# Kernel tuning notes

Hardware: AMD Instinct MI355X
Metric: run time of the kernel (lower is better)

Reference implementation:

```python
import jax, jax.numpy as jnp
import numpy as np

DIM = 512      # model dim
HEADS = 8      # attention heads
WS = 256       # window_size
G = 32         # num_global_tokens
SPARSITY = 0.3 # fraction of entries masked out per row by the sparsity controller


def setup_inputs() -> dict:
    key = jax.random.key(0)
    ks = jax.random.split(key, 7)
    b, n = 4, 8192
    x = jax.random.normal(ks[0], (b, n, DIM), dtype=jnp.float32)
    w_qkv = jax.random.normal(ks[1], (DIM, 3 * DIM), dtype=jnp.float32) * (DIM ** -0.5)
    w_out = jax.random.normal(ks[2], (DIM, DIM), dtype=jnp.float32) * (DIM ** -0.5)
    b_out = jnp.zeros((DIM,), dtype=jnp.float32)
    local_bias = jax.random.normal(ks[3], (HEADS, WS, WS), dtype=jnp.float32)
    global_param = jax.random.normal(ks[4], (HEADS, G, WS), dtype=jnp.float32)
    gate = jax.random.normal(ks[5], (HEADS,), dtype=jnp.float32)
    return {"x": x, "w_qkv": w_qkv, "w_out": w_out, "b_out": b_out,
            "local_bias": local_bias, "global_param": global_param, "gate": gate}


def reference(x, w_qkv, w_out, b_out, local_bias, global_param, gate):
    b, n, _ = x.shape
    h, ws, g = HEADS, WS, G
    d = DIM // h
    w = n // ws  # number of windows
    scale = DIM ** -0.5

    qkv = x @ w_qkv                      # [b, n, 3*dim]
    q, k, v = jnp.split(qkv, 3, axis=-1)

    def to_win(t):  # [b, n, dim] -> [b, h, w, ws, d]
        return t.reshape(b, n, h, d).transpose(0, 2, 1, 3).reshape(b, h, w, ws, d)

    q, k, v = to_win(q), to_win(k), to_win(v)

    # windowed local attention with learned per-window additive bias
    local = jnp.einsum('bhwnd,bhwmd->bhwnm', q, k) * scale   # [b,h,w,ws,ws]
    local = local + local_bias[None, :, None]                # bias broadcast over b, w

    # global-token attention term built from window-averaged q/k
    q_mean = q.mean(axis=2)  # [b,h,ws,d]
    k_mean = k.mean(axis=2)  # [b,h,ws,d]
    global_q = jnp.einsum('hgn,bhnd->bhgd', global_param, q_mean)      # [b,h,g,d]
    global_scores = jnp.einsum('bhgd,bhmd->bhgm', global_q, k_mean) * scale  # [b,h,g,ws]
    global_bias = global_scores.mean(axis=2)                            # [b,h,ws]

    # sparsity controller: learned per-head gate combines local + global,
    # then top-k row sparsification keeps (1-sparsity) of entries pre-softmax
    gate_h = jax.nn.sigmoid(gate)[None, :, None, None, None]
    scores = local + gate_h * global_bias[:, :, None, None, :]          # [b,h,w,ws,ws]
    k_keep = int(ws * (1.0 - SPARSITY))
    thresh = jax.lax.top_k(scores, k_keep)[0][..., -1:]                 # kth largest per row
    scores = jnp.where(scores >= thresh, scores, jnp.float32(-1e9))

    attn = jax.nn.softmax(scores, axis=-1)
    out = jnp.einsum('bhwnm,bhwmd->bhwnd', attn, v)                     # [b,h,w,ws,d]
    out = out.reshape(b, h, n, d).transpose(0, 2, 1, 3).reshape(b, n, DIM)
    return out @ w_out + b_out
```

## Files before the change

### kernel.cpp

```cpp
#include <hip/hip_runtime.h>

#define NN    8192
#define WSZ   256
#define KKEEP 179
#define SCALE 0.044194173824159216f

typedef __attribute__((ext_vector_type(8))) __bf16 bf16x8;
typedef __attribute__((ext_vector_type(4))) short  s16x4;
typedef __attribute__((ext_vector_type(8))) short  s16x8;
typedef __attribute__((ext_vector_type(4))) float  f32x4;

struct Split3 { short h, m, l; };
__device__ __forceinline__ Split3 split3(float x)
{
    unsigned u  = __float_as_uint(x);
    unsigned hb = ((u + 0x7FFFu + ((u >> 16) & 1u)) >> 16) << 16;
    float r = x - __uint_as_float(hb);
    unsigned ur = __float_as_uint(r);
    unsigned mb = ((ur + 0x7FFFu + ((ur >> 16) & 1u)) >> 16) << 16;
    float r2 = r - __uint_as_float(mb);
    unsigned lr = __float_as_uint(r2);
    unsigned lb = (lr + 0x7FFFu + ((lr >> 16) & 1u)) >> 16;
    Split3 s;
    s.h = (short)(hb >> 16);
    s.m = (short)(mb >> 16);
    s.l = (short)(lb & 0xFFFFu);
    return s;
}

__global__ __launch_bounds__(256) void splitw_kernel(const float* __restrict__ W,
                                                     int K, int N,
                                                     short* __restrict__ h,
                                                     short* __restrict__ m,
                                                     short* __restrict__ l)
{
    int idx = blockIdx.x * 256 + threadIdx.x;
    if (idx >= K * N) return;
    int k = idx / N, n = idx - k * N;
    Split3 s = split3(W[idx]);
    size_t o = (size_t)n * K + k;
    h[o] = s.h; m[o] = s.m; l[o] = s.l;
}

__global__ __launch_bounds__(256, 2) void gemm_mfma(const float* __restrict__ A, int lda,
                                                    const short* __restrict__ BTh,
                                                    const short* __restrict__ BTm,
                                                    const short* __restrict__ BTl,
                                                    const float* __restrict__ bias,
                                                    float* __restrict__ C, int ldc,
                                                    int qk_cols)
{
    __shared__ __align__(16) short Asm[3][128 * 40];
    __shared__ __align__(16) short Bsm[3][128 * 40];

    const int t       = threadIdx.x;
    const int lane    = t & 63;
    const int wave    = t >> 6;
    const int wr      = wave >> 1;
    const int wc      = wave & 1;
    const int rowBase = blockIdx.y * 128;
    const int colBase = blockIdx.x * 128;
    const int pstart  = (colBase < qk_cols) ? 0 : 3;

    const int sa[6] = {2, 0, 1, 1, 0, 0};
    const int sb[6] = {0, 2, 1, 0, 1, 0};

    const int fn = lane & 15;
    const int fq = (lane >> 4) * 8;

    f32x4 acc[4][4] = {};

    for (int ks = 0; ks < 512; ks += 32) {
        __syncthreads();

#pragma unroll
        for (int lo = 0; lo < 4; ++lo) {
            int idx = lo * 256 + t;
            int am  = idx >> 3;
            int af  = (idx & 7) * 4;
            float4 a4 = *(const float4*)&A[(size_t)(rowBase + am) * lda + ks + af];
            Split3 s0 = split3(a4.x);
            Split3 s1 = split3(a4.y);
            Split3 s2 = split3(a4.z);
            Split3 s3 = split3(a4.w);
            s16x4 hv, mv, lv;
            hv[0] = s0.h; hv[1] = s1.h; hv[2] = s2.h; hv[3] = s3.h;
            mv[0] = s0.m; mv[1] = s1.m; mv[2] = s2.m; mv[3] = s3.m;
            lv[0] = s0.l; lv[1] = s1.l; lv[2] = s2.l; lv[3] = s3.l;
            int o = am * 40 + af;
            *(s16x4*)&Asm[0][o] = hv;
            *(s16x4*)&Asm[1][o] = mv;
            *(s16x4*)&Asm[2][o] = lv;
        }
#pragma unroll
        for (int lo = 0; lo < 2; ++lo) {
            int c = lo * 256 + t;
            int n = c >> 2;
            int q = (c & 3) * 8;
            size_t src = (size_t)(colBase + n) * 512 + ks + q;
            int o = n * 40 + q;
            *(s16x8*)&Bsm[0][o] = *(const s16x8*)&BTh[src];
            *(s16x8*)&Bsm[1][o] = *(const s16x8*)&BTm[src];
            *(s16x8*)&Bsm[2][o] = *(const s16x8*)&BTl[src];
        }
        __syncthreads();

        bf16x8 Bf[3][4];
#pragma unroll
        for (int s = 0; s < 3; ++s)
#pragma unroll
            for (int j = 0; j < 4; ++j)
                Bf[s][j] = *(const bf16x8*)&Bsm[s][(wc * 64 + j * 16 + fn) * 40 + fq];

#pragma unroll
        for (int i = 0; i < 4; ++i) {
            bf16x8 Af[3];
#pragma unroll
            for (int s = 0; s < 3; ++s)
                Af[s] = *(const bf16x8*)&Asm[s][(wr * 64 + i * 16 + fn) * 40 + fq];
#pragma unroll
            for (int p = 0; p < 6; ++p) {
                if (p < pstart) continue;
#pragma unroll
                for (int j = 0; j < 4; ++j)
                    acc[i][j] = __builtin_amdgcn_mfma_f32_16x16x32_bf16(
                        Af[sa[p]], Bf[sb[p]][j], acc[i][j], 0, 0, 0);
            }
        }
    }

    const int crow0 = rowBase + wr * 64 + (lane >> 4) * 4;
    const int ccol0 = colBase + wc * 64 + fn;
#pragma unroll
    for (int j = 0; j < 4; ++j) {
        int col = ccol0 + j * 16;
        float bv = bias ? bias[col] : 0.0f;
#pragma unroll
        for (int i = 0; i < 4; ++i)
#pragma unroll
            for (int r = 0; r < 4; ++r)
                C[(size_t)(crow0 + i * 16 + r) * ldc + col] = acc[i][j][r] + bv;
    }
}

__global__ __launch_bounds__(256) void means_kernel(const float* __restrict__ qkv,
                                                    float* __restrict__ q_mean,
                                                    float* __restrict__ k_mean)
{
    int idx = blockIdx.x * 256 + threadIdx.x;
    int dd = idx & 63;
    int i  = (idx >> 6) & 255;
    int bh = idx >> 14;
    int b = bh >> 3, h = bh & 7;
    const float* base = qkv + (size_t)b * NN * 1536 + (size_t)h * 64 + dd;
    float qs = 0.f, ks = 0.f;
#pragma unroll
    for (int w = 0; w < 32; ++w) {
        size_t off = (size_t)(w * 256 + i) * 1536;
        qs += base[off];
        ks += base[off + 512];
    }
    q_mean[idx] = qs * 0.03125f;
    k_mean[idx] = ks * 0.03125f;
}

__global__ __launch_bounds__(256) void globalbias_kernel(const float* __restrict__ q_mean,
                                                         const float* __restrict__ k_mean,
                                                         const float* __restrict__ gp,
                                                         float* __restrict__ gbias)
{
    __shared__ float gq[32 * 64];
    const int bh = blockIdx.x;
    const int h  = bh & 7;
    const int t  = threadIdx.x;

#pragma unroll
    for (int e = 0; e < 8; ++e) {
        int idx = e * 256 + t;
        int g  = idx >> 6;
        int dd = idx & 63;
        const float* gpr = gp + (size_t)(h * 32 + g) * 256;
        const float* qm  = q_mean + (size_t)bh * 16384 + dd;
        float s = 0.f;
        for (int i = 0; i < 256; ++i) s += gpr[i] * qm[(size_t)i * 64];
        gq[idx] = s;
    }
    __syncthreads();

    const float* km = k_mean + (size_t)bh * 16384 + (size_t)t * 64;
    float4 kr[16];
#pragma unroll
    for (int j = 0; j < 16; ++j) kr[j] = *(const float4*)&km[4 * j];
    float acc = 0.f;
    for (int g = 0; g < 32; ++g) {
        const float* gqr = &gq[g * 64];
        float s = 0.f;
#pragma unroll
        for (int j = 0; j < 16; ++j) {
            float4 q4 = *(const float4*)&gqr[4 * j];
            s += q4.x * kr[j].x + q4.y * kr[j].y + q4.z * kr[j].z + q4.w * kr[j].w;
        }
        acc += s;
    }
    gbias[bh * 256 + t] = acc * SCALE * 0.03125f;
}

__device__ __forceinline__ unsigned mono_enc(float f) {
    unsigned u = __float_as_uint(f);
    return (u & 0x80000000u) ? ~u : (u | 0x80000000u);
}
__device__ __forceinline__ float mono_dec(unsigned e) {
    return (e & 0x80000000u) ? __uint_as_float(e ^ 0x80000000u)
                             : __uint_as_float(~e);
}

__global__ __launch_bounds__(256, 3) void attn_kernel(float* __restrict__ qkv,
                                                      const float* __restrict__ local_bias,
                                                      const float* __restrict__ gbias,
                                                      const float* __restrict__ gate)
{
    __shared__ float qT[64 * 68];
    __shared__ float kT[64 * 68];
    __shared__ float st[64 * 68];

    const int t   = threadIdx.x;
    const int blk = blockIdx.x;
    const int rc  = blk & 3;
    const int w   = (blk >> 2) & 31;
    const int bh  = blk >> 7;
    const int h   = bh & 7;
    const int b   = bh >> 3;
    const float gateh = 1.0f / (1.0f + __expf(-gate[h]));

    const size_t tokBase = (size_t)b * NN + (size_t)w * WSZ;
    float* qb = qkv + tokBase * 1536 + h * 64;
    const float* kb = qb + 512;
    const float* vb = qb + 1024;

    const int tr = t >> 4, tc = t & 15;
    const int rr = t >> 2, sub = t & 3;

#pragma unroll
    for (int l = 0; l < 4; ++l) {
        int f  = l * 256 + t;
        int r  = f >> 4;
        int dg = (f & 15) * 4;
        float4 v4 = *(const float4*)&qb[(size_t)(rc * 64 + r) * 1536 + dg];
        int cs = (r + dg) & 63;
        qT[(dg + 0) * 68 + cs] = v4.x;
        qT[(dg + 1) * 68 + cs] = v4.y;
        qT[(dg + 2) * 68 + cs] = v4.z;
        qT[(dg + 3) * 68 + cs] = v4.w;
    }

    float vals[64];
#pragma unroll
    for (int mc = 0; mc < 4; ++mc) {
        __syncthreads();
#pragma unroll
        for (int l = 0; l < 4; ++l) {
            int f  = l * 256 + t;
            int m  = f >> 4;
            int dg = (f & 15) * 4;
            float4 v4 = *(const float4*)&kb[(size_t)(mc * 64 + m) * 1536 + dg];
            int cs = (m + dg) & 63;
            kT[(dg + 0) * 68 + cs] = v4.x;
            kT[(dg + 1) * 68 + cs] = v4.y;
            kT[(dg + 2) * 68 + cs] = v4.z;
            kT[(dg + 3) * 68 + cs] = v4.w;
        }
        __syncthreads();

        float acc[4][4] = {};
#pragma unroll 8
        for (int d = 0; d < 64; ++d) {
            int sw = d & 60;
            float4 q4 = *(const float4*)&qT[d * 68 + ((4 * tr + sw) & 63)];
            float4 k4 = *(const float4*)&kT[d * 68 + ((4 * tc + sw) & 63)];
            float qa[4] = {q4.x, q4.y, q4.z, q4.w};
            float ka[4] = {k4.x, k4.y, k4.z, k4.w};
#pragma unroll
            for (int i = 0; i < 4; ++i)
#pragma unroll
                for (int j = 0; j < 4; ++j)
                    acc[i][j] += qa[i] * ka[j];
        }
        float4 gb4 = *(const float4*)&gbias[bh * 256 + mc * 64 + 4 * tc];
        float gbl[4] = {gb4.x, gb4.y, gb4.z, gb4.w};
#pragma unroll
        for (int i = 0; i < 4; ++i) {
            int row = rc * 64 + 4 * tr + i;
            float4 lb4 = *(const float4*)&local_bias[((size_t)h * 256 + row) * 256 + mc * 64 + 4 * tc];
            float4 o;
            o.x = acc[i][0] * SCALE + lb4.x + gateh * gbl[0];
            o.y = acc[i][1] * SCALE + lb4.y + gateh * gbl[1];
            o.z = acc[i][2] * SCALE + lb4.z + gateh * gbl[2];
            o.w = acc[i][3] * SCALE + lb4.w + gateh * gbl[3];
            *(float4*)&st[(4 * tr + i) * 68 + 4 * tc] = o;
        }
        __syncthreads();
#pragma unroll
        for (int j = 0; j < 16; ++j)
            vals[mc * 16 + j] = st[rr * 68 + sub + 4 * j];
    }

    float rmin = vals[0], rmax = vals[0];
#pragma unroll
    for (int j = 1; j < 64; ++j) {
        rmin = fminf(rmin, vals[j]);
        rmax = fmaxf(rmax, vals[j]);
    }
    rmin = fminf(rmin, __shfl_xor(rmin, 1)); rmin = fminf(rmin, __shfl_xor(rmin, 2));
    rmax = fmaxf(rmax, __shfl_xor(rmax, 1)); rmax = fmaxf(rmax, __shfl_xor(rmax, 2));

    float flo = rmin, fhi = rmax;
    float thr = 0.f;
    bool  done = false;
    for (int it = 0; it < 16; ++it) {
        if (__all(done ? 1 : 0)) break;
        float mf = 0.5f * (flo + fhi);
        int c = 0;
#pragma unroll
        for (int j = 0; j < 64; ++j) c += (vals[j] >= mf) ? 1 : 0;
        c += __shfl_xor(c, 1);
        c += __shfl_xor(c, 2);
        if (!done) {
            if (c == KKEEP)      { thr = mf; done = true; }
            else if (c > KKEEP)  flo = mf;
            else                 fhi = mf;
        }
    }
    if (__any(done ? 0 : 1)) {
        unsigned lo_u = mono_enc(flo), hi_u = mono_enc(fhi);
        for (int it = 0; it < 34; ++it) {
            bool active = (!done) && (lo_u < hi_u);
            if (!__any(active ? 1 : 0)) break;
            unsigned span = hi_u - lo_u;
            unsigned mid  = lo_u + (span >> 1) + (span & 1u);
            float mf = mono_dec(mid);
            int c = 0;
#pragma unroll
            for (int j = 0; j < 64; ++j) c += (vals[j] >= mf) ? 1 : 0;
            c += __shfl_xor(c, 1);
            c += __shfl_xor(c, 2);
            if (active) {
                if (c == KKEEP)      { thr = mf; done = true; }
                else if (c >= KKEEP) lo_u = mid;
                else                 hi_u = mid - 1;
            }
        }
        if (!done) thr = mono_dec(lo_u);
    }

    float rmx = -3e38f;
#pragma unroll
    for (int j = 0; j < 64; ++j) rmx = fmaxf(rmx, (vals[j] >= thr) ? vals[j] : -3e38f);
    rmx = fmaxf(rmx, __shfl_xor(rmx, 1));
    rmx = fmaxf(rmx, __shfl_xor(rmx, 2));
    float rsum = 0.f;
#pragma unroll
    for (int j = 0; j < 64; ++j) {
        float e = (vals[j] >= thr) ? __expf(vals[j] - rmx) : 0.f;
        vals[j] = e;
        rsum += e;
    }
    rsum += __shfl_xor(rsum, 1);
    rsum += __shfl_xor(rsum, 2);
    float rinv = 1.0f / rsum;
#pragma unroll
    for (int j = 0; j < 64; ++j) vals[j] *= rinv;

    float acc2[4][4] = {};
#pragma unroll
    for (int mc = 0; mc < 4; ++mc) {
        __syncthreads();
#pragma unroll
        for (int j = 0; j < 16; ++j)
            st[(sub + 4 * j) * 68 + rr] = vals[mc * 16 + j];
#pragma unroll
        for (int l = 0; l < 4; ++l) {
            int f  = l * 256 + t;
            int m  = f >> 4;
            int dg = (f & 15) * 4;
            *(float4*)&kT[m * 68 + dg] =
                *(const float4*)&vb[(size_t)(mc * 64 + m) * 1536 + dg];
        }
        __syncthreads();
#pragma unroll 8
        for (int m = 0; m < 64; ++m) {
            float4 p4 = *(const float4*)&st[m * 68 + 4 * tr];
            float4 v4 = *(const float4*)&kT[m * 68 + 4 * tc];
            float pa[4] = {p4.x, p4.y, p4.z, p4.w};
            float va[4] = {v4.x, v4.y, v4.z, v4.w};
#pragma unroll
            for (int i = 0; i < 4; ++i)
#pragma unroll
                for (int j = 0; j < 4; ++j)
                    acc2[i][j] += pa[i] * va[j];
        }
    }

#pragma unroll
    for (int i = 0; i < 4; ++i) {
        float4 o;
        o.x = acc2[i][0]; o.y = acc2[i][1]; o.z = acc2[i][2]; o.w = acc2[i][3];
        *(float4*)&qb[(size_t)(rc * 64 + 4 * tr + i) * 1536 + 4 * tc] = o;
    }
}

extern "C" void kernel_launch(void* const* d_in, const int* in_sizes, int n_in,
                              void* d_out, int out_size, void* d_ws, size_t ws_size,
                              hipStream_t stream)
{
    (void)in_sizes; (void)n_in; (void)out_size; (void)ws_size;
    const float* x            = (const float*)d_in[0];
    const float* w_qkv        = (const float*)d_in[1];
    const float* w_out        = (const float*)d_in[2];
    const float* b_out        = (const float*)d_in[3];
    const float* local_bias   = (const float*)d_in[4];
    const float* global_param = (const float*)d_in[5];
    const float* gate         = (const float*)d_in[6];
    float* out = (float*)d_out;
    float* ws  = (float*)d_ws;

    float* qkv    = ws;
    float* q_mean = qkv + (size_t)32768 * 1536;
    float* k_mean = q_mean + (size_t)32 * 256 * 64;
    float* gb     = k_mean + (size_t)32 * 256 * 64;
    short* wsp    = (short*)(gb + 8192);
    short* WTh  = wsp;
    short* WTm  = WTh + (size_t)1536 * 512;
    short* WTl  = WTm + (size_t)1536 * 512;
    short* WoTh = WTl + (size_t)1536 * 512;
    short* WoTm = WoTh + (size_t)512 * 512;
    short* WoTl = WoTm + (size_t)512 * 512;

    splitw_kernel<<<3072, 256, 0, stream>>>(w_qkv, 512, 1536, WTh, WTm, WTl);
    splitw_kernel<<<1024, 256, 0, stream>>>(w_out, 512, 512, WoTh, WoTm, WoTl);
    gemm_mfma<<<dim3(12, 256), 256, 0, stream>>>(x, 512, WTh, WTm, WTl,
                                                 nullptr, qkv, 1536, 1024);
    means_kernel<<<2048, 256, 0, stream>>>(qkv, q_mean, k_mean);
    globalbias_kernel<<<32, 256, 0, stream>>>(q_mean, k_mean, global_param, gb);
    attn_kernel<<<4096, 256, 0, stream>>>(qkv, local_bias, gb, gate);
    gemm_mfma<<<dim3(4, 256), 256, 0, stream>>>(qkv, 1536, WoTh, WoTm, WoTl,
                                                b_out, out, 512, 0);
}
```

Baseline: 857.1 us.

## Use split-bf16 MFMA for QK^T and PV in attention kernel

After: 740.3 us. 13.6% less time.

```diff
diff --git a/kernel.cpp b/kernel.cpp
--- a/kernel.cpp
+++ b/kernel.cpp
@@ -26,6 +26,17 @@
     s.m = (short)(mb >> 16);
     s.l = (short)(lb & 0xFFFFu);
     return s;
+}
+
+__device__ __forceinline__ void split2(float x, short& h, short& m)
+{
+    unsigned u  = __float_as_uint(x);
+    unsigned hb = ((u + 0x7FFFu + ((u >> 16) & 1u)) >> 16) << 16;
+    float r = x - __uint_as_float(hb);
+    unsigned ur = __float_as_uint(r);
+    unsigned mb = (ur + 0x7FFFu + ((ur >> 16) & 1u)) >> 16;
+    h = (short)(hb >> 16);
+    m = (short)(mb & 0xFFFFu);
 }
 
 __global__ __launch_bounds__(256) void splitw_kernel(const float* __restrict__ W,
@@ -219,11 +230,19 @@
                                                       const float* __restrict__ gbias,
                                                       const float* __restrict__ gate)
 {
-    __shared__ float qT[64 * 68];
-    __shared__ float kT[64 * 68];
-    __shared__ float st[64 * 68];
-
-    const int t   = threadIdx.x;
+    __shared__ __align__(16) short Qs[3 * 64 * 64];
+    __shared__ __align__(16) short Ks[3 * 64 * 64];
+    float* st = (float*)(void*)Ks;
+
+    const int t    = threadIdx.x;
+    const int lane = t & 63;
+    const int wave = t >> 6;
+    const int wr   = wave >> 1;
+    const int wc   = wave & 1;
+    const int fn   = lane & 15;
+    const int fq   = (lane >> 4) * 8;
+    const int g4   = (lane >> 4) * 4;
+
     const int blk = blockIdx.x;
     const int rc  = blk & 3;
     const int w   = (blk >> 2) & 31;
@@ -237,20 +256,26 @@
     const float* kb = qb + 512;
     const float* vb = qb + 1024;
 
-    const int tr = t >> 4, tc = t & 15;
     const int rr = t >> 2, sub = t & 3;
+
+    const int sa[6] = {2, 0, 1, 1, 0, 0};
+    const int sb[6] = {0, 2, 1, 0, 1, 0};
 
 #pragma unroll
     for (int l = 0; l < 4; ++l) {
         int f  = l * 256 + t;
         int r  = f >> 4;
         int dg = (f & 15) * 4;
-        float4 v4 = *(const float4*)&qb[(size_t)(rc * 64 + r) * 1536 + dg];
-        int cs = (r + dg) & 63;
-        qT[(dg + 0) * 68 + cs] = v4.x;
-        qT[(dg + 1) * 68 + cs] = v4.y;
-        qT[(dg + 2) * 68 + cs] = v4.z;
-        qT[(dg + 3) * 68 + cs] = v4.w;
+        float4 a4 = *(const float4*)&qb[(size_t)(rc * 64 + r) * 1536 + dg];
+        Split3 s0 = split3(a4.x), s1 = split3(a4.y), s2 = split3(a4.z), s3 = split3(a4.w);
+        s16x4 hv, mv, lv;
+        hv[0] = s0.h; hv[1] = s1.h; hv[2] = s2.h; hv[3] = s3.h;
+        mv[0] = s0.m; mv[1] = s1.m; mv[2] = s2.m; mv[3] = s3.m;
+        lv[0] = s0.l; lv[1] = s1.l; lv[2] = s2.l; lv[3] = s3.l;
+        int o = r * 64 + (dg ^ ((r & 7) << 3));
+        *(s16x4*)&Qs[o]        = hv;
+        *(s16x4*)&Qs[4096 + o] = mv;
+        *(s16x4*)&Qs[8192 + o] = lv;
     }
 
     float vals[64];
@@ -262,41 +287,56 @@
             int f  = l * 256 + t;
             int m  = f >> 4;
             int dg = (f & 15) * 4;
-            float4 v4 = *(const float4*)&kb[(size_t)(mc * 64 + m) * 1536 + dg];
-            int cs = (m + dg) & 63;
-            kT[(dg + 0) * 68 + cs] = v4.x;
-            kT[(dg + 1) * 68 + cs] = v4.y;
-            kT[(dg + 2) * 68 + cs] = v4.z;
-            kT[(dg + 3) * 68 + cs] = v4.w;
-        }
-        __syncthreads();
-
-        float acc[4][4] = {};
-#pragma unroll 8
-        for (int d = 0; d < 64; ++d) {
-            int sw = d & 60;
-            float4 q4 = *(const float4*)&qT[d * 68 + ((4 * tr + sw) & 63)];
-            float4 k4 = *(const float4*)&kT[d * 68 + ((4 * tc + sw) & 63)];
-            float qa[4] = {q4.x, q4.y, q4.z, q4.w};
-            float ka[4] = {k4.x, k4.y, k4.z, k4.w};
-#pragma unroll
-            for (int i = 0; i < 4; ++i)
-#pragma unroll
-                for (int j = 0; j < 4; ++j)
-                    acc[i][j] += qa[i] * ka[j];
-        }
-        float4 gb4 = *(const float4*)&gbias[bh * 256 + mc * 64 + 4 * tc];
-        float gbl[4] = {gb4.x, gb4.y, gb4.z, gb4.w};
-#pragma unroll
-        for (int i = 0; i < 4; ++i) {
-            int row = rc * 64 + 4 * tr + i;
-            float4 lb4 = *(const float4*)&local_bias[((size_t)h * 256 + row) * 256 + mc * 64 + 4 * tc];
-            float4 o;
-            o.x = acc[i][0] * SCALE + lb4.x + gateh * gbl[0];
-            o.y = acc[i][1] * SCALE + lb4.y + gateh * gbl[1];
-            o.z = acc[i][2] * SCALE + lb4.z + gateh * gbl[2];
-            o.w = acc[i][3] * SCALE + lb4.w + gateh * gbl[3];
-            *(float4*)&st[(4 * tr + i) * 68 + 4 * tc] = o;
+            float4 a4 = *(const float4*)&kb[(size_t)(mc * 64 + m) * 1536 + dg];
+            Split3 s0 = split3(a4.x), s1 = split3(a4.y), s2 = split3(a4.z), s3 = split3(a4.w);
+            s16x4 hv, mv, lv;
+            hv[0] = s0.h; hv[1] = s1.h; hv[2] = s2.h; hv[3] = s3.h;
+            mv[0] = s0.m; mv[1] = s1.m; mv[2] = s2.m; mv[3] = s3.m;
+            lv[0] = s0.l; lv[1] = s1.l; lv[2] = s2.l; lv[3] = s3.l;
+            int o = m * 64 + (dg ^ ((m & 7) << 3));
+            *(s16x4*)&Ks[o]        = hv;
+            *(s16x4*)&Ks[4096 + o] = mv;
+            *(s16x4*)&Ks[8192 + o] = lv;
+        }
+        __syncthreads();
+
+        f32x4 acc[2][2] = {};
+#pragma unroll
+        for (int kk = 0; kk < 2; ++kk) {
+            bf16x8 Af[3][2], Bf[3][2];
+#pragma unroll
+            for (int s = 0; s < 3; ++s)
+#pragma unroll
+                for (int i = 0; i < 2; ++i) {
+                    int ar = wr * 32 + i * 16 + fn;
+                    int bc = wc * 32 + i * 16 + fn;
+                    Af[s][i] = *(const bf16x8*)&Qs[s * 4096 + ar * 64 + ((kk * 32 + fq) ^ ((ar & 7) << 3))];
+                    Bf[s][i] = *(const bf16x8*)&Ks[s * 4096 + bc * 64 + ((kk * 32 + fq) ^ ((bc & 7) << 3))];
+                }
+#pragma unroll
+            for (int p = 0; p < 6; ++p)
+#pragma unroll
+                for (int i = 0; i < 2; ++i)
+#pragma unroll
+                    for (int j = 0; j < 2; ++j)
+                        acc[i][j] = __builtin_amdgcn_mfma_f32_16x16x32_bf16(
+                            Af[sa[p]][i], Bf[sb[p]][j], acc[i][j], 0, 0, 0);
+        }
+        __syncthreads();
+
+#pragma unroll
+        for (int j = 0; j < 2; ++j) {
+            int cl = wc * 32 + j * 16 + fn;
+            int cf = mc * 64 + cl;
+            float gb = gateh * gbias[bh * 256 + cf];
+#pragma unroll
+            for (int i = 0; i < 2; ++i)
+#pragma unroll
+                for (int r = 0; r < 4; ++r) {
+                    int rl = wr * 32 + i * 16 + g4 + r;
+                    st[rl * 68 + cl] = acc[i][j][r] * SCALE
+                        + local_bias[((size_t)h * 256 + rc * 64 + rl) * 256 + cf] + gb;
+                }
         }
         __syncthreads();
 #pragma unroll
@@ -370,42 +410,72 @@
 #pragma unroll
     for (int j = 0; j < 64; ++j) vals[j] *= rinv;
 
-    float acc2[4][4] = {};
+    const int sa2[3] = {1, 0, 0};
+    const int sb2[3] = {0, 1, 0};
+    f32x4 acc2[2][2] = {};
 #pragma unroll
     for (int mc = 0; mc < 4; ++mc) {
         __syncthreads();
 #pragma unroll
-        for (int j = 0; j < 16; ++j)
-            st[(sub + 4 * j) * 68 + rr] = vals[mc * 16 + j];
-#pragma unroll
-        for (int l = 0; l < 4; ++l) {
+        for (int u = 0; u < 16; ++u) {
+            short ph, pm;
+            split2(vals[mc * 16 + u], ph, pm);
+            int ml   = sub + 4 * u;
+            int slot = rr * 64 + (ml ^ ((rr & 7) << 3));
+            Qs[slot]        = ph;
+            Qs[4096 + slot] = pm;
+        }
+#pragma unroll
+        for (int l = 0; l < 2; ++l) {
             int f  = l * 256 + t;
-            int m  = f >> 4;
-            int dg = (f & 15) * 4;
-            *(float4*)&kT[m * 68 + dg] =
-                *(const float4*)&vb[(size_t)(mc * 64 + m) * 1536 + dg];
-        }
-        __syncthreads();
-#pragma unroll 8
-        for (int m = 0; m < 64; ++m) {
-            float4 p4 = *(const float4*)&st[m * 68 + 4 * tr];
-            float4 v4 = *(const float4*)&kT[m * 68 + 4 * tc];
-            float pa[4] = {p4.x, p4.y, p4.z, p4.w};
-            float va[4] = {v4.x, v4.y, v4.z, v4.w};
-#pragma unroll
-            for (int i = 0; i < 4; ++i)
-#pragma unroll
-                for (int j = 0; j < 4; ++j)
-                    acc2[i][j] += pa[i] * va[j];
-        }
-    }
-
-#pragma unroll
-    for (int i = 0; i < 4; ++i) {
-        float4 o;
-        o.x = acc2[i][0]; o.y = acc2[i][1]; o.z = acc2[i][2]; o.w = acc2[i][3];
-        *(float4*)&qb[(size_t)(rc * 64 + 4 * tr + i) * 1536 + 4 * tc] = o;
-    }
+            int d  = f & 63;
+            int mo = (f >> 6) * 8;
+            s16x8 hv, mv;
+#pragma unroll
+            for (int i = 0; i < 8; ++i) {
+                short vh, vm;
+                split2(vb[(size_t)(mc * 64 + mo + i) * 1536 + d], vh, vm);
+                hv[i] = vh; mv[i] = vm;
+            }
+            int o = d * 72 + mo;
+            *(s16x8*)&Ks[o]        = hv;
+            *(s16x8*)&Ks[4608 + o] = mv;
+        }
+        __syncthreads();
+
+#pragma unroll
+        for (int kk = 0; kk < 2; ++kk) {
+            bf16x8 Pf[2][2], Vf[2][2];
+#pragma unroll
+            for (int s = 0; s < 2; ++s)
+#pragma unroll
+                for (int i = 0; i < 2; ++i) {
+                    int pr = wr * 32 + i * 16 + fn;
+                    int dr = wc * 32 + i * 16 + fn;
+                    Pf[s][i] = *(const bf16x8*)&Qs[s * 4096 + pr * 64 + ((kk * 32 + fq) ^ ((pr & 7) << 3))];
+                    Vf[s][i] = *(const bf16x8*)&Ks[s * 4608 + dr * 72 + kk * 32 + fq];
+                }
+#pragma unroll
+            for (int p = 0; p < 3; ++p)
+#pragma unroll
+                for (int i = 0; i < 2; ++i)
+#pragma unroll
+                    for (int j = 0; j < 2; ++j)
+                        acc2[i][j] = __builtin_amdgcn_mfma_f32_16x16x32_bf16(
+                            Pf[sa2[p]][i], Vf[sb2[p]][j], acc2[i][j], 0, 0, 0);
+        }
+    }
+
+#pragma unroll
+    for (int j = 0; j < 2; ++j)
+#pragma unroll
+        for (int i = 0; i < 2; ++i)
+#pragma unroll
+            for (int r = 0; r < 4; ++r) {
+                int row = rc * 64 + wr * 32 + i * 16 + g4 + r;
+                int d   = wc * 32 + j * 16 + fn;
+                qb[(size_t)row * 1536 + d] = acc2[i][j][r];
+            }
 }
 
 extern "C" void kernel_launch(void* const* d_in, const int* in_sizes, int n_in,
```
